# Optimization experiments

Hardware: AMD Instinct MI355X
Metric: run time of the kernel (lower is better)

## Reference

```python
import jax, jax.numpy as jnp
import numpy as np

B, LP, LE, D, H, DK, DV, DF = 16, 2047, 2048, 1024, 16, 64, 64, 4096


def _layer_norm(x, g, b, eps=1e-5):
    m = x.mean(-1, keepdims=True)
    v = ((x - m) ** 2).mean(-1, keepdims=True)
    return (x - m) * jax.lax.rsqrt(v + eps) * g + b


def _mha(q, kv, wq, wk, wv, wo, bo, g, b):
    # q: [B,Q,D], kv: [B,L,D]; per-head projections wq/wk: [H,D,DK], wv: [H,D,DV]
    residual = q
    Q = jnp.einsum('bqd,hdk->bhqk', q, wq)
    K = jnp.einsum('bld,hdk->bhlk', kv, wk)
    V = jnp.einsum('bld,hdv->bhlv', kv, wv)
    scale = jnp.sqrt(jnp.asarray(Q.shape[-1], Q.dtype))
    attn = jax.nn.softmax(jnp.einsum('bhqk,bhlk->bhql', Q, K) / scale, axis=-1)
    o = jnp.einsum('bhql,bhlv->bhqv', attn, V)
    o = o.transpose(0, 2, 1, 3).reshape(q.shape[0], q.shape[1], -1)  # concat heads
    o = o @ wo + bo
    return _layer_norm(o + residual, g, b), attn


def setup_inputs() -> dict:
    key = jax.random.key(0)
    ks = jax.random.split(key, 16)
    s = 0.02
    inp = {
        'dec_input': jax.random.normal(ks[0], (B, 1, D), jnp.float32),
        'input_history': jax.random.normal(ks[1], (B, LP, D), jnp.float32),
        'enc_output': jax.random.normal(ks[2], (B, LE, D), jnp.float32),
        'wq_s': jax.random.normal(ks[3], (H, D, DK), jnp.float32) * s,
        'wk_s': jax.random.normal(ks[4], (H, D, DK), jnp.float32) * s,
        'wv_s': jax.random.normal(ks[5], (H, D, DV), jnp.float32) * s,
        'wo_s': jax.random.normal(ks[6], (H * DV, D), jnp.float32) * s,
        'bo_s': jnp.zeros((D,), jnp.float32),
        'ln1_g': jnp.ones((D,), jnp.float32),
        'ln1_b': jnp.zeros((D,), jnp.float32),
        'wq_c': jax.random.normal(ks[7], (H, D, DK), jnp.float32) * s,
        'wk_c': jax.random.normal(ks[8], (H, D, DK), jnp.float32) * s,
        'wv_c': jax.random.normal(ks[9], (H, D, DV), jnp.float32) * s,
        'wo_c': jax.random.normal(ks[10], (H * DV, D), jnp.float32) * s,
        'bo_c': jnp.zeros((D,), jnp.float32),
        'ln2_g': jnp.ones((D,), jnp.float32),
        'ln2_b': jnp.zeros((D,), jnp.float32),
        'ffn_w1': jax.random.normal(ks[11], (D, DF), jnp.float32) * s,
        'ffn_b1': jnp.zeros((DF,), jnp.float32),
        'ffn_w2': jax.random.normal(ks[12], (DF, D), jnp.float32) * s,
        'ffn_b2': jnp.zeros((D,), jnp.float32),
        'ln3_g': jnp.ones((D,), jnp.float32),
        'ln3_b': jnp.zeros((D,), jnp.float32),
    }
    return inp


def reference(dec_input, input_history, enc_output,
              wq_s, wk_s, wv_s, wo_s, bo_s, ln1_g, ln1_b,
              wq_c, wk_c, wv_c, wo_c, bo_c, ln2_g, ln2_b,
              ffn_w1, ffn_b1, ffn_w2, ffn_b2, ln3_g, ln3_b):
    # KV-cache growth: history <- cat(history, dec_input)
    history = jnp.concatenate([input_history, dec_input], axis=1)  # [B, LP+1, D]
    x, slf_attn = _mha(dec_input, history, wq_s, wk_s, wv_s, wo_s, bo_s, ln1_g, ln1_b)
    x, enc_attn = _mha(x, enc_output, wq_c, wk_c, wv_c, wo_c, bo_c, ln2_g, ln2_b)
    y = jax.nn.relu(x @ ffn_w1 + ffn_b1) @ ffn_w2 + ffn_b2
    out = _layer_norm(y + x, ln3_g, ln3_b)
    return (out, slf_attn, enc_attn)
```

## Files before the change

### kernel.cpp

```cpp
#include <hip/hip_runtime.h>
#include <hip/hip_bf16.h>
#include <stdint.h>
#include <stddef.h>


#define DEV __device__ __forceinline__

typedef __attribute__((ext_vector_type(8))) short bf16x8;
typedef __attribute__((ext_vector_type(4))) short bf16x4;
typedef __attribute__((ext_vector_type(4))) float f32x4;

DEV unsigned short f2b(float f){
  union { __hip_bfloat16 h; unsigned short u; } cv;
  cv.h = __float2bfloat16(f);
  return cv.u;
}
DEV float b2f(unsigned short u){
  union { unsigned int i; float f; } cv;
  cv.i = ((unsigned int)u) << 16;
  return cv.f;
}
DEV f32x4 mfma16(bf16x8 a, bf16x8 b, f32x4 c){
  return __builtin_amdgcn_mfma_f32_16x16x32_bf16(a, b, c, 0, 0, 0);
}

__global__ __launch_bounds__(256) void g_qp2(const float* __restrict__ src,
    const float* __restrict__ wq, const float* __restrict__ wk,
    unsigned short* __restrict__ qpb){
  int u = blockIdx.x, b = u >> 4, h = u & 15;
  int t = threadIdx.x;
  __shared__ float red[256];
  __shared__ float Qs[64];
  {
    int k = t & 63, q = t >> 6;
    const float* s = src + (size_t)b*1024 + q*256;
    const float* w = wq + (size_t)h*65536 + (size_t)(q*256)*64 + k;
    float a0=0.f,a1=0.f,a2=0.f,a3=0.f;
    for(int d=0; d<256; d+=4){
      a0 += s[d]   * w[(size_t)d*64];
      a1 += s[d+1] * w[(size_t)(d+1)*64];
      a2 += s[d+2] * w[(size_t)(d+2)*64];
      a3 += s[d+3] * w[(size_t)(d+3)*64];
    }
    red[t] = a0+a1+a2+a3;
    __syncthreads();
    if(t < 64) Qs[t] = (red[t]+red[t+64]+red[t+128]+red[t+192])*0.125f;
    __syncthreads();
  }
  for(int i=0;i<4;++i){
    int d = t + i*256;
    const float* w = wk + ((size_t)h*1024 + d)*64;
    float acc = 0.f;
    #pragma unroll
    for(int k4=0;k4<16;++k4){
      float4 wv4 = *(const float4*)(w + k4*4);
      acc += wv4.x*Qs[k4*4] + wv4.y*Qs[k4*4+1] + wv4.z*Qs[k4*4+2] + wv4.w*Qs[k4*4+3];
    }
    qpb[(size_t)u*1024 + d] = f2b(acc);
  }
}

__global__ __launch_bounds__(256) void g_attn(const float* __restrict__ kvsrc,
    const float* __restrict__ decrow, const unsigned short* __restrict__ qpb,
    float* __restrict__ scr, unsigned short* __restrict__ partb,
    float* __restrict__ msum, int lsrc){
  int u = blockIdx.x, ns = u & 63, b = u >> 6;
  int t = threadIdx.x, lane = t & 63, w = t >> 6;
  int r = lane & 15, hi = lane >> 4;
  int slice0 = ns*32;

  __shared__ unsigned short lt[1024*20];
  __shared__ float red[1024];
  __shared__ unsigned short p_lds[16*40];
  __shared__ float f_lds[16];

  float4 ld[16];
  auto ISSUE = [&](int c){
    int row = slice0 + c*16 + r;
    const float* rp = (row < lsrc) ? kvsrc + ((size_t)b*lsrc + row)*1024
                                   : decrow + (size_t)b*1024;
    rp += w*256 + hi*8;
    #pragma unroll
    for(int kk=0; kk<8; ++kk){
      ld[kk*2+0] = *(const float4*)(rp + kk*32);
      ld[kk*2+1] = *(const float4*)(rp + kk*32 + 4);
    }
  };

  ISSUE(0);
  for(int i=t; i<16*40; i+=256) p_lds[i] = 0;

  bf16x8 qf[8];
  {
    const unsigned short* qp = qpb + ((size_t)b*16 + r)*1024 + w*256 + hi*8;
    #pragma unroll
    for(int kk=0;kk<8;++kk) qf[kk] = *(const bf16x8*)(qp + kk*32);
  }

  f32x4 acc[16];
  #pragma unroll
  for(int i=0;i<16;++i) acc[i] = (f32x4){0.f,0.f,0.f,0.f};
  float m_run = -1e30f, s_run = 0.f;

  __syncthreads();
  for(int c=0; c<2; ++c){
    f32x4 s_acc = {0.f,0.f,0.f,0.f};
    int colw = r ^ ((hi & 1) << 3);
    #pragma unroll
    for(int kk=0; kk<8; ++kk){
      float4 a0 = ld[kk*2], a1 = ld[kk*2+1];
      bf16x8 v;
      v[0]=(short)f2b(a0.x); v[1]=(short)f2b(a0.y);
      v[2]=(short)f2b(a0.z); v[3]=(short)f2b(a0.w);
      v[4]=(short)f2b(a1.x); v[5]=(short)f2b(a1.y);
      v[6]=(short)f2b(a1.z); v[7]=(short)f2b(a1.w);
      unsigned short* pt = &lt[(w*256 + hi*8 + kk*32)*20 + colw];
      #pragma unroll
      for(int j=0;j<8;++j) pt[j*20] = (unsigned short)v[j];
      s_acc = mfma16(v, qf[kk], s_acc);
    }
    if(c < 1) ISSUE(c+1);
    *(f32x4*)&red[t*4] = s_acc;
    __syncthreads();

    f32x4 ss = *(const f32x4*)&red[(0*64+lane)*4];
    ss += *(const f32x4*)&red[(1*64+lane)*4];
    ss += *(const f32x4*)&red[(2*64+lane)*4];
    ss += *(const f32x4*)&red[(3*64+lane)*4];
    float sf[4] = {ss[0], ss[1], ss[2], ss[3]};
    float mc = fmaxf(fmaxf(sf[0],sf[1]), fmaxf(sf[2],sf[3]));
    mc = fmaxf(mc, __shfl_xor(mc, 16));
    mc = fmaxf(mc, __shfl_xor(mc, 32));
    float nm = fmaxf(m_run, mc);
    float fch = __expf(m_run - nm);
    float pvv[4]; float ps = 0.f;
    #pragma unroll
    for(int i=0;i<4;++i){ pvv[i] = __expf(sf[i]-nm); ps += pvv[i]; }
    ps += __shfl_xor(ps, 16);
    ps += __shfl_xor(ps, 32);
    s_run = s_run*fch + ps;
    m_run = nm;
    if(w == 0){
      #pragma unroll
      for(int i=0;i<4;++i) p_lds[r*40 + hi*4 + i] = f2b(pvv[i]);
      if(hi == 0) f_lds[r] = fch;
      float* sp = scr + ((size_t)b*16 + r)*2048 + slice0 + c*16 + hi*4;
      *(float4*)sp = (float4){sf[0], sf[1], sf[2], sf[3]};
    }
    __syncthreads();

    f32x4 fv = *(const f32x4*)&f_lds[hi*4];
    bf16x8 pa = *(const bf16x8*)&p_lds[r*40 + hi*8];
    #pragma unroll
    for(int dc=0; dc<16; ++dc){
      acc[dc] *= fv;
      int d = w*256 + dc*16 + r;
      int col0 = (((hi & 1) ^ ((r >> 3) & 1)) << 3);
      bf16x4 blo = *(const bf16x4*)&lt[d*20 + col0];
      bf16x4 bhi = *(const bf16x4*)&lt[d*20 + col0 + 4];
      bf16x8 bv;
      bv[0]=blo[0]; bv[1]=blo[1]; bv[2]=blo[2]; bv[3]=blo[3];
      bv[4]=bhi[0]; bv[5]=bhi[1]; bv[6]=bhi[2]; bv[7]=bhi[3];
      acc[dc] = mfma16(pa, bv, acc[dc]);
    }
    __syncthreads();
  }
  unsigned short* pl = lt;
  #pragma unroll
  for(int dc=0; dc<16; ++dc)
    #pragma unroll
    for(int i=0;i<4;++i)
      pl[(hi*4+i)*1024 + w*256 + dc*16 + r] = f2b(acc[dc][i]);
  __syncthreads();
  {
    const uint4* s4 = (const uint4*)pl;
    uint4* d4 = (uint4*)(partb + (((size_t)b*64 + ns)*16)*1024);
    #pragma unroll
    for(int j=0;j<8;++j) d4[t + j*256] = s4[t + j*256];
  }
  if(w==0 && hi==0){
    msum[(((size_t)b*64 + ns)*16 + r)*2 + 0] = m_run;
    msum[(((size_t)b*64 + ns)*16 + r)*2 + 1] = s_run;
  }
}

__global__ __launch_bounds__(256) void g_fin(const unsigned short* __restrict__ partb,
    const float* __restrict__ msum, const float* __restrict__ scr,
    const float* __restrict__ wv, const float* __restrict__ wo,
    float* __restrict__ attn_out, float* __restrict__ gpart){
  int u = blockIdx.x, b = u >> 4, h = u & 15;
  int t = threadIdx.x;
  __shared__ float marr[64], earr[64], ctxs[1024], red2[256], obh[64];
  if(t < 64){
    marr[t] = msum[(((size_t)b*64 + t)*16 + h)*2 + 0];
    earr[t] = msum[(((size_t)b*64 + t)*16 + h)*2 + 1];
  }
  __syncthreads();
  float M = -1e30f;
  for(int i=0;i<64;++i) M = fmaxf(M, marr[i]);
  float SUM = 0.f;
  for(int i=0;i<64;++i) SUM += __expf(marr[i]-M)*earr[i];
  float inv = 1.f/SUM;
  __syncthreads();
  if(t < 64) earr[t] = __expf(marr[t]-M)*inv;
  __syncthreads();
  {
    const unsigned short* pb0 = partb + ((size_t)b*64*16 + h)*1024 + t*4;
    float ax=0.f, ay=0.f, az=0.f, aw=0.f;
    for(int nsq=0; nsq<64; ++nsq){
      ushort4 uu = *(const ushort4*)(pb0 + (size_t)nsq*16384);
      float e = earr[nsq];
      ax += e*b2f(uu.x); ay += e*b2f(uu.y); az += e*b2f(uu.z); aw += e*b2f(uu.w);
    }
    *(float4*)&ctxs[t*4] = (float4){ax,ay,az,aw};
  }
  const float* sp = scr + ((size_t)b*16 + h)*2048;
  float* po = attn_out + ((size_t)b*16 + h)*2048;
  #pragma unroll
  for(int i=0;i<8;++i){ int l = t + i*256; po[l] = __expf(sp[l]-M)*inv; }
  __syncthreads();
  int v = t & 63, q = t >> 6;
  const float* wp = wv + ((size_t)h*1024 + q*256)*64 + v;
  float a0=0.f,a1=0.f,a2=0.f,a3=0.f;
  for(int dd=0; dd<256; dd+=4){
    a0 += ctxs[q*256+dd]   * wp[(size_t)dd*64];
    a1 += ctxs[q*256+dd+1] * wp[(size_t)(dd+1)*64];
    a2 += ctxs[q*256+dd+2] * wp[(size_t)(dd+2)*64];
    a3 += ctxs[q*256+dd+3] * wp[(size_t)(dd+3)*64];
  }
  red2[t] = a0+a1+a2+a3;
  __syncthreads();
  if(t < 64) obh[t] = red2[t]+red2[t+64]+red2[t+128]+red2[t+192];
  __syncthreads();
  float accn[4] = {0.f,0.f,0.f,0.f};
  const float* wrow = wo + (size_t)h*64*1024;
  for(int vv=0; vv<64; ++vv){
    float s = obh[vv];
    const float* wr = wrow + (size_t)vv*1024;
    #pragma unroll
    for(int i=0;i<4;++i) accn[i] += s * wr[t + i*256];
  }
  #pragma unroll
  for(int i=0;i<4;++i) gpart[((size_t)h*16 + b)*1024 + t + i*256] = accn[i];
}

__global__ __launch_bounds__(256) void g_ln(const float* __restrict__ parts, int KS,
    const float* __restrict__ bias, const float* __restrict__ resid,
    const float* __restrict__ g, const float* __restrict__ bb,
    float* __restrict__ xout, unsigned short* __restrict__ xb16){
  int b = blockIdx.x, t = threadIdx.x;
  __shared__ float red[256];
  const float4* bias4  = (const float4*)bias;
  const float4* resid4 = (const float4*)resid + (size_t)b*256;
  const float4* parts4 = (const float4*)parts;
  float4 s = bias4[t];
  { float4 rr = resid4[t]; s.x+=rr.x; s.y+=rr.y; s.z+=rr.z; s.w+=rr.w; }
  #pragma unroll 4
  for(int k=0;k<KS;++k){
    float4 pp = parts4[((size_t)k*16 + b)*256 + t];
    s.x+=pp.x; s.y+=pp.y; s.z+=pp.z; s.w+=pp.w;
  }
  red[t] = s.x+s.y+s.z+s.w; __syncthreads();
  for(int off=128; off>0; off>>=1){ if(t<off) red[t]+=red[t+off]; __syncthreads(); }
  float mean = red[0]*(1.f/1024.f); __syncthreads();
  float dx=s.x-mean, dy=s.y-mean, dz=s.z-mean, dw=s.w-mean;
  red[t] = dx*dx+dy*dy+dz*dz+dw*dw; __syncthreads();
  for(int off=128; off>0; off>>=1){ if(t<off) red[t]+=red[t+off]; __syncthreads(); }
  float rstd = rsqrtf(red[0]*(1.f/1024.f) + 1e-5f);
  float4 g4 = ((const float4*)g)[t], b4 = ((const float4*)bb)[t];
  float4 y;
  y.x = dx*rstd*g4.x + b4.x;
  y.y = dy*rstd*g4.y + b4.y;
  y.z = dz*rstd*g4.z + b4.z;
  y.w = dw*rstd*g4.w + b4.w;
  if(xout) ((float4*)xout)[(size_t)b*256 + t] = y;
  if(xb16){
    ushort4 uu;
    uu.x = f2b(y.x); uu.y = f2b(y.y); uu.z = f2b(y.z); uu.w = f2b(y.w);
    ((ushort4*)xb16)[(size_t)b*256 + t] = uu;
  }
}

__global__ __launch_bounds__(256) void g_skg(const float* __restrict__ W,
    const unsigned short* __restrict__ A, float* __restrict__ part,
    int N, int K, int KS){
  int nt = blockIdx.x, ks = blockIdx.y;
  int Ksl = K / KS, k0b = ks * Ksl, n0 = nt*64;
  int nc = Ksl >> 5;
  __shared__ unsigned short lt[2][64*40];
  int t = threadIdx.x, lane = t & 63, w = t >> 6;
  int k_loc = t >> 3, n_off = (t & 7)*8;
  const unsigned short* apb = A + (size_t)(lane & 15)*K + (lane >> 4)*8 + k0b;
  f32x4 acc = {0.f,0.f,0.f,0.f};
  float4 x0, x1;
  auto LD = [&](int c){
    const float* wp = W + (size_t)(k0b + c*32 + k_loc)*N + n0 + n_off;
    x0 = *(const float4*)wp;
    x1 = *(const float4*)(wp + 4);
  };
  auto ST = [&](int buf){
    unsigned short* p = &lt[buf][0];
    p[(n_off+0)*40 + k_loc] = f2b(x0.x);
    p[(n_off+1)*40 + k_loc] = f2b(x0.y);
    p[(n_off+2)*40 + k_loc] = f2b(x0.z);
    p[(n_off+3)*40 + k_loc] = f2b(x0.w);
    p[(n_off+4)*40 + k_loc] = f2b(x1.x);
    p[(n_off+5)*40 + k_loc] = f2b(x1.y);
    p[(n_off+6)*40 + k_loc] = f2b(x1.z);
    p[(n_off+7)*40 + k_loc] = f2b(x1.w);
  };
  LD(0); ST(0);
  for(int c=0; c<nc; ++c){
    if(c+1 < nc) LD(c+1);
    __syncthreads();
    bf16x8 af = *(const bf16x8*)(apb + c*32);
    bf16x8 bv = *(const bf16x8*)&lt[c&1][(w*16 + (lane & 15))*40 + (lane >> 4)*8];
    acc = mfma16(af, bv, acc);
    if(c+1 < nc) ST((c+1)&1);
  }
  int col = n0 + w*16 + (lane & 15);
  int r0 = (lane >> 4)*4;
  #pragma unroll
  for(int i=0;i<4;++i)
    part[ ((size_t)ks*16 + r0 + i)*(size_t)N + col ] = acc[i];
}

__global__ __launch_bounds__(256) void g_relu(const float* __restrict__ parts, int KS,
    const float* __restrict__ b1, unsigned short* __restrict__ h1){
  int i = blockIdx.x*256 + threadIdx.x;
  int b = i >> 10, f4 = i & 1023;
  float4 s = ((const float4*)b1)[f4];
  #pragma unroll 4
  for(int k=0;k<KS;++k){
    float4 pp = ((const float4*)parts)[((size_t)k*16 + b)*1024 + f4];
    s.x+=pp.x; s.y+=pp.y; s.z+=pp.z; s.w+=pp.w;
  }
  ushort4 uu;
  uu.x = f2b(fmaxf(s.x,0.f)); uu.y = f2b(fmaxf(s.y,0.f));
  uu.z = f2b(fmaxf(s.z,0.f)); uu.w = f2b(fmaxf(s.w,0.f));
  ((ushort4*)h1)[i] = uu;
}

extern "C" void kernel_launch(void* const* d_in, const int* in_sizes, int n_in,
                              void* d_out, int out_size, void* d_ws, size_t ws_size,
                              hipStream_t stream){
  const float* dec    = (const float*)d_in[0];
  const float* hist   = (const float*)d_in[1];
  const float* enc    = (const float*)d_in[2];
  const float* wq_s   = (const float*)d_in[3];
  const float* wk_s   = (const float*)d_in[4];
  const float* wv_s   = (const float*)d_in[5];
  const float* wo_s   = (const float*)d_in[6];
  const float* bo_s   = (const float*)d_in[7];
  const float* ln1_g  = (const float*)d_in[8];
  const float* ln1_b  = (const float*)d_in[9];
  const float* wq_c   = (const float*)d_in[10];
  const float* wk_c   = (const float*)d_in[11];
  const float* wv_c   = (const float*)d_in[12];
  const float* wo_c   = (const float*)d_in[13];
  const float* bo_c   = (const float*)d_in[14];
  const float* ln2_g  = (const float*)d_in[15];
  const float* ln2_b  = (const float*)d_in[16];
  const float* w1     = (const float*)d_in[17];
  const float* b1     = (const float*)d_in[18];
  const float* w2     = (const float*)d_in[19];
  const float* b2     = (const float*)d_in[20];
  const float* ln3_g  = (const float*)d_in[21];
  const float* ln3_b  = (const float*)d_in[22];

  float* out  = (float*)d_out;
  float* slf  = out + 16384;
  float* enco = out + 16384 + 524288;

  char* w = (char*)d_ws;
  float*          scr    = (float*)(w + 0x0000000);
  unsigned short* partb  = (unsigned short*)(w + 0x0200000);
  float*          msum   = (float*)(w + 0x2200000);
  unsigned short* qpb    = (unsigned short*)(w + 0x2240000);
  float*          x1     = (float*)(w + 0x22C0000);
  float*          x2     = (float*)(w + 0x22D0000);
  unsigned short* x2b    = (unsigned short*)(w + 0x22E0000);
  unsigned short* h1b    = (unsigned short*)(w + 0x22F0000);
  float*          gpart  = (float*)(w + 0x2400000);
  float*          fpart  = (float*)(w + 0x2500000);
  float*          g2part = (float*)(w + 0x2700000);

  g_qp2 <<<256,  256, 0, stream>>>(dec, wq_s, wk_s, qpb);
  g_attn<<<1024, 256, 0, stream>>>(hist, dec, qpb, scr, partb, msum, 2047);
  g_fin <<<256,  256, 0, stream>>>(partb, msum, scr, wv_s, wo_s, slf, gpart);
  g_ln  <<<16,   256, 0, stream>>>(gpart, 16, bo_s, dec, ln1_g, ln1_b, x1, (unsigned short*)0);

  g_qp2 <<<256,  256, 0, stream>>>(x1, wq_c, wk_c, qpb);
  g_attn<<<1024, 256, 0, stream>>>(enc, dec, qpb, scr, partb, msum, 2048);
  g_fin <<<256,  256, 0, stream>>>(partb, msum, scr, wv_c, wo_c, enco, gpart);
  g_ln  <<<16,   256, 0, stream>>>(gpart, 16, bo_c, x1, ln2_g, ln2_b, x2, x2b);

  g_skg <<<dim3(64,8),  256, 0, stream>>>(w1, x2b, fpart, 4096, 1024, 8);
  g_relu<<<64,  256, 0, stream>>>(fpart, 8, b1, h1b);
  g_skg <<<dim3(16,32), 256, 0, stream>>>(w2, h1b, g2part, 1024, 4096, 32);
  g_ln  <<<16,  256, 0, stream>>>(g2part, 32, b2, x2, ln3_g, ln3_b, out, (unsigned short*)0);
}
```

Before: 194.7 us.

## Split attention finalize into combine, MFMA V-projection, reduction and output GEMM

Replaces the monolithic g_fin kernel, where each (batch, head) block did scalar fp32 V and output projections, with four stages. A wider combine kernel merges the partial contexts and writes the softmax rows. An MFMA-based V-projection batches all 16 batch rows per head, and a small reduction collects its split-K partials. The output projection reuses the existing split-K bf16 GEMM. The aim is more parallelism and tensor-core throughput in place of serial per-block weight streaming, at the cost of extra launches, intermediate traffic and bf16 rounding of the context and projected values.

```diff
diff --git a/kernel.cpp b/kernel.cpp
--- a/kernel.cpp
+++ b/kernel.cpp
@@ -77,13 +77,13 @@
   float4 ld[16];
   auto ISSUE = [&](int c){
     int row = slice0 + c*16 + r;
-    const float* rp = (row < lsrc) ? kvsrc + ((size_t)b*lsrc + row)*1024
-                                   : decrow + (size_t)b*1024;
-    rp += w*256 + hi*8;
+    const float* rpp = (row < lsrc) ? kvsrc + ((size_t)b*lsrc + row)*1024
+                                    : decrow + (size_t)b*1024;
+    rpp += w*256 + hi*8;
     #pragma unroll
     for(int kk=0; kk<8; ++kk){
-      ld[kk*2+0] = *(const float4*)(rp + kk*32);
-      ld[kk*2+1] = *(const float4*)(rp + kk*32 + 4);
+      ld[kk*2+0] = *(const float4*)(rpp + kk*32);
+      ld[kk*2+1] = *(const float4*)(rpp + kk*32 + 4);
     }
   };
 
@@ -184,64 +184,93 @@
   }
 }
 
-__global__ __launch_bounds__(256) void g_fin(const unsigned short* __restrict__ partb,
-    const float* __restrict__ msum, const float* __restrict__ scr,
-    const float* __restrict__ wv, const float* __restrict__ wo,
-    float* __restrict__ attn_out, float* __restrict__ gpart){
-  int u = blockIdx.x, b = u >> 4, h = u & 15;
+__global__ __launch_bounds__(256) void g_comb(const float* __restrict__ msum,
+    const float* __restrict__ scr, const unsigned short* __restrict__ partb,
+    float* __restrict__ attn_out, unsigned short* __restrict__ ctxb){
+  int dq = blockIdx.x, bh = blockIdx.y, b = bh >> 4, h = bh & 15;
   int t = threadIdx.x;
-  __shared__ float marr[64], earr[64], ctxs[1024], red2[256], obh[64];
+  __shared__ float e_lds[64];
+  __shared__ float Mi[2];
   if(t < 64){
-    marr[t] = msum[(((size_t)b*64 + t)*16 + h)*2 + 0];
-    earr[t] = msum[(((size_t)b*64 + t)*16 + h)*2 + 1];
+    float2 ms = *(const float2*)&msum[(((size_t)b*64 + t)*16 + h)*2];
+    float M = ms.x;
+    #pragma unroll
+    for(int o=1; o<64; o<<=1) M = fmaxf(M, __shfl_xor(M, o));
+    float e = __expf(ms.x - M)*ms.y;
+    float S = e;
+    #pragma unroll
+    for(int o=1; o<64; o<<=1) S += __shfl_xor(S, o);
+    e_lds[t] = __expf(ms.x - M)/S;
+    if(t == 0){ Mi[0] = M; Mi[1] = 1.f/S; }
   }
   __syncthreads();
-  float M = -1e30f;
-  for(int i=0;i<64;++i) M = fmaxf(M, marr[i]);
-  float SUM = 0.f;
-  for(int i=0;i<64;++i) SUM += __expf(marr[i]-M)*earr[i];
-  float inv = 1.f/SUM;
-  __syncthreads();
-  if(t < 64) earr[t] = __expf(marr[t]-M)*inv;
-  __syncthreads();
-  {
-    const unsigned short* pb0 = partb + ((size_t)b*64*16 + h)*1024 + t*4;
-    float ax=0.f, ay=0.f, az=0.f, aw=0.f;
-    for(int nsq=0; nsq<64; ++nsq){
-      ushort4 uu = *(const ushort4*)(pb0 + (size_t)nsq*16384);
-      float e = earr[nsq];
-      ax += e*b2f(uu.x); ay += e*b2f(uu.y); az += e*b2f(uu.z); aw += e*b2f(uu.w);
-    }
-    *(float4*)&ctxs[t*4] = (float4){ax,ay,az,aw};
-  }
-  const float* sp = scr + ((size_t)b*16 + h)*2048;
-  float* po = attn_out + ((size_t)b*16 + h)*2048;
+  float M = Mi[0], inv = Mi[1];
+  const float* sp = scr + (size_t)bh*2048 + dq*512;
+  float* po = attn_out + (size_t)bh*2048 + dq*512;
+  po[t]     = __expf(sp[t]     - M)*inv;
+  po[t+256] = __expf(sp[t+256] - M)*inv;
+  int d = dq*256 + t;
+  const unsigned short* pb0 = partb + ((size_t)b*64*16 + h)*1024 + d;
+  float acc = 0.f;
+  #pragma unroll 8
+  for(int ns=0; ns<64; ++ns)
+    acc += e_lds[ns]*b2f(pb0[(size_t)ns*16384]);
+  ctxb[(size_t)bh*1024 + d] = f2b(acc);
+}
+
+__global__ __launch_bounds__(256) void g_vproj(const float* __restrict__ wv,
+    const unsigned short* __restrict__ ctxb, float* __restrict__ opart){
+  int ks = blockIdx.x, h = blockIdx.y;
+  int k0b = ks*128;
+  __shared__ unsigned short lt[2][64*40];
+  int t = threadIdx.x, lane = t & 63, w = t >> 6;
+  int k_loc = t >> 3, n_off = (t & 7)*8;
+  const unsigned short* apb = ctxb + (size_t)(lane & 15)*16384 + (size_t)h*1024
+                              + (lane >> 4)*8 + k0b;
+  const float* Wb = wv + (size_t)h*65536;
+  f32x4 acc = {0.f,0.f,0.f,0.f};
+  float4 x0, x1;
+  auto LD = [&](int c){
+    const float* wp = Wb + (size_t)(k0b + c*32 + k_loc)*64 + n_off;
+    x0 = *(const float4*)wp;
+    x1 = *(const float4*)(wp + 4);
+  };
+  auto ST = [&](int buf){
+    unsigned short* p = &lt[buf][0];
+    p[(n_off+0)*40 + k_loc] = f2b(x0.x);
+    p[(n_off+1)*40 + k_loc] = f2b(x0.y);
+    p[(n_off+2)*40 + k_loc] = f2b(x0.z);
+    p[(n_off+3)*40 + k_loc] = f2b(x0.w);
+    p[(n_off+4)*40 + k_loc] = f2b(x1.x);
+    p[(n_off+5)*40 + k_loc] = f2b(x1.y);
+    p[(n_off+6)*40 + k_loc] = f2b(x1.z);
+    p[(n_off+7)*40 + k_loc] = f2b(x1.w);
+  };
+  LD(0); ST(0);
+  for(int c=0; c<4; ++c){
+    if(c+1 < 4) LD(c+1);
+    __syncthreads();
+    bf16x8 af = *(const bf16x8*)(apb + c*32);
+    bf16x8 bv = *(const bf16x8*)&lt[c&1][(w*16 + (lane & 15))*40 + (lane >> 4)*8];
+    acc = mfma16(af, bv, acc);
+    if(c+1 < 4) ST((c+1)&1);
+  }
+  int col = w*16 + (lane & 15);
+  int r0 = (lane >> 4)*4;
   #pragma unroll
-  for(int i=0;i<8;++i){ int l = t + i*256; po[l] = __expf(sp[l]-M)*inv; }
-  __syncthreads();
-  int v = t & 63, q = t >> 6;
-  const float* wp = wv + ((size_t)h*1024 + q*256)*64 + v;
-  float a0=0.f,a1=0.f,a2=0.f,a3=0.f;
-  for(int dd=0; dd<256; dd+=4){
-    a0 += ctxs[q*256+dd]   * wp[(size_t)dd*64];
-    a1 += ctxs[q*256+dd+1] * wp[(size_t)(dd+1)*64];
-    a2 += ctxs[q*256+dd+2] * wp[(size_t)(dd+2)*64];
-    a3 += ctxs[q*256+dd+3] * wp[(size_t)(dd+3)*64];
-  }
-  red2[t] = a0+a1+a2+a3;
-  __syncthreads();
-  if(t < 64) obh[t] = red2[t]+red2[t+64]+red2[t+128]+red2[t+192];
-  __syncthreads();
-  float accn[4] = {0.f,0.f,0.f,0.f};
-  const float* wrow = wo + (size_t)h*64*1024;
-  for(int vv=0; vv<64; ++vv){
-    float s = obh[vv];
-    const float* wr = wrow + (size_t)vv*1024;
-    #pragma unroll
-    for(int i=0;i<4;++i) accn[i] += s * wr[t + i*256];
-  }
+  for(int i=0;i<4;++i)
+    opart[ ((size_t)(h*8 + ks)*16 + r0 + i)*64 + col ] = acc[i];
+}
+
+__global__ __launch_bounds__(256) void g_ovred(const float* __restrict__ opart,
+    unsigned short* __restrict__ ob){
+  int i = blockIdx.x*256 + threadIdx.x;
+  int b = i >> 10, hv = i & 1023, h = hv >> 6, v = hv & 63;
+  float s = 0.f;
   #pragma unroll
-  for(int i=0;i<4;++i) gpart[((size_t)h*16 + b)*1024 + t + i*256] = accn[i];
+  for(int ks=0; ks<8; ++ks)
+    s += opart[ ((size_t)(h*8 + ks)*16 + b)*64 + v ];
+  ob[(size_t)b*1024 + hv] = f2b(s);
 }
 
 __global__ __launch_bounds__(256) void g_ln(const float* __restrict__ parts, int KS,
@@ -377,26 +406,35 @@
   unsigned short* partb  = (unsigned short*)(w + 0x0200000);
   float*          msum   = (float*)(w + 0x2200000);
   unsigned short* qpb    = (unsigned short*)(w + 0x2240000);
-  float*          x1     = (float*)(w + 0x22C0000);
-  float*          x2     = (float*)(w + 0x22D0000);
-  unsigned short* x2b    = (unsigned short*)(w + 0x22E0000);
-  unsigned short* h1b    = (unsigned short*)(w + 0x22F0000);
-  float*          gpart  = (float*)(w + 0x2400000);
-  float*          fpart  = (float*)(w + 0x2500000);
-  float*          g2part = (float*)(w + 0x2700000);
-
-  g_qp2 <<<256,  256, 0, stream>>>(dec, wq_s, wk_s, qpb);
-  g_attn<<<1024, 256, 0, stream>>>(hist, dec, qpb, scr, partb, msum, 2047);
-  g_fin <<<256,  256, 0, stream>>>(partb, msum, scr, wv_s, wo_s, slf, gpart);
-  g_ln  <<<16,   256, 0, stream>>>(gpart, 16, bo_s, dec, ln1_g, ln1_b, x1, (unsigned short*)0);
-
-  g_qp2 <<<256,  256, 0, stream>>>(x1, wq_c, wk_c, qpb);
-  g_attn<<<1024, 256, 0, stream>>>(enc, dec, qpb, scr, partb, msum, 2048);
-  g_fin <<<256,  256, 0, stream>>>(partb, msum, scr, wv_c, wo_c, enco, gpart);
-  g_ln  <<<16,   256, 0, stream>>>(gpart, 16, bo_c, x1, ln2_g, ln2_b, x2, x2b);
-
-  g_skg <<<dim3(64,8),  256, 0, stream>>>(w1, x2b, fpart, 4096, 1024, 8);
-  g_relu<<<64,  256, 0, stream>>>(fpart, 8, b1, h1b);
-  g_skg <<<dim3(16,32), 256, 0, stream>>>(w2, h1b, g2part, 1024, 4096, 32);
-  g_ln  <<<16,  256, 0, stream>>>(g2part, 32, b2, x2, ln3_g, ln3_b, out, (unsigned short*)0);
-}
+  unsigned short* ctxb   = (unsigned short*)(w + 0x22C0000);
+  float*          opart  = (float*)(w + 0x2340000);
+  unsigned short* ob     = (unsigned short*)(w + 0x23C0000);
+  float*          x1     = (float*)(w + 0x23D0000);
+  float*          x2     = (float*)(w + 0x23E0000);
+  unsigned short* x2b    = (unsigned short*)(w + 0x23F0000);
+  unsigned short* h1b    = (unsigned short*)(w + 0x2400000);
+  float*          gpart  = (float*)(w + 0x2500000);
+  float*          fpart  = (float*)(w + 0x2600000);
+  float*          g2part = (float*)(w + 0x2800000);
+
+  g_qp2  <<<256,  256, 0, stream>>>(dec, wq_s, wk_s, qpb);
+  g_attn <<<1024, 256, 0, stream>>>(hist, dec, qpb, scr, partb, msum, 2047);
+  g_comb <<<dim3(4,256), 256, 0, stream>>>(msum, scr, partb, slf, ctxb);
+  g_vproj<<<dim3(8,16),  256, 0, stream>>>(wv_s, ctxb, opart);
+  g_ovred<<<64,   256, 0, stream>>>(opart, ob);
+  g_skg  <<<dim3(16,16), 256, 0, stream>>>(wo_s, ob, gpart, 1024, 1024, 16);
+  g_ln   <<<16,   256, 0, stream>>>(gpart, 16, bo_s, dec, ln1_g, ln1_b, x1, (unsigned short*)0);
+
+  g_qp2  <<<256,  256, 0, stream>>>(x1, wq_c, wk_c, qpb);
+  g_attn <<<1024, 256, 0, stream>>>(enc, dec, qpb, scr, partb, msum, 2048);
+  g_comb <<<dim3(4,256), 256, 0, stream>>>(msum, scr, partb, enco, ctxb);
+  g_vproj<<<dim3(8,16),  256, 0, stream>>>(wv_c, ctxb, opart);
+  g_ovred<<<64,   256, 0, stream>>>(opart, ob);
+  g_skg  <<<dim3(16,16), 256, 0, stream>>>(wo_c, ob, gpart, 1024, 1024, 16);
+  g_ln   <<<16,   256, 0, stream>>>(gpart, 16, bo_c, x1, ln2_g, ln2_b, x2, x2b);
+
+  g_skg  <<<dim3(64,8),  256, 0, stream>>>(w1, x2b, fpart, 4096, 1024, 8);
+  g_relu <<<64,  256, 0, stream>>>(fpart, 8, b1, h1b);
+  g_skg  <<<dim3(16,32), 256, 0, stream>>>(w2, h1b, g2part, 1024, 4096, 32);
+  g_ln   <<<16,  256, 0, stream>>>(g2part, 32, b2, x2, ln3_g, ln3_b, out, (unsigned short*)0);
+}
```

Result: no change. 196.8 us (+1.1%).
